# Performance work log

Hardware: AMD Instinct MI355X
Metric: run time of the kernel (lower is better)

## Reference

```python
import jax, jax.numpy as jnp
import numpy as np

NEG_SLOPE_GAT = 0.2   # GATv2 attention LeakyReLU slope (PyG default)
NEG_SLOPE_ACT = 0.01  # nn.LeakyReLU() default slope in outer module
LN_EPS = 1e-5
SOFTMAX_EPS = 1e-16   # PyG softmax denominator epsilon

B, C, N = 2, 128, 50000
H, FH = 2, 64          # heads=2, out_channels=64 -> concat dim 128
E = 800000
M = B * N


def setup_inputs() -> dict:
    key = jax.random.key(0)
    ks = jax.random.split(key, 10)
    s_in = 1.0 / np.sqrt(C)
    s_att = 1.0 / np.sqrt(FH)
    return {
        "x": jax.random.normal(ks[0], (B, C, N, 1), jnp.float32),
        "edge_index": jax.random.randint(ks[1], (2, E), 0, M, jnp.int32),
        "W_l": jax.random.normal(ks[2], (C, H * FH), jnp.float32) * s_in,
        "b_l": jnp.zeros((H * FH,), jnp.float32),
        "W_r": jax.random.normal(ks[3], (C, H * FH), jnp.float32) * s_in,
        "b_r": jnp.zeros((H * FH,), jnp.float32),
        "att": jax.random.normal(ks[4], (H, FH), jnp.float32) * s_att,
        "bias_gat": jnp.zeros((H * FH,), jnp.float32),
        "gamma": jnp.ones((H * FH,), jnp.float32),
        "beta": jnp.zeros((H * FH,), jnp.float32),
    }


def reference(x, edge_index, W_l, b_l, W_r, b_r, att, bias_gat, gamma, beta):
    Bx, Cx, Nx, _ = x.shape
    Mn = Bx * Nx
    # x.squeeze(3).permute(0,2,1).reshape(-1, C)  -> (B*N, C) node features
    xn = jnp.transpose(x[..., 0], (0, 2, 1)).reshape(Mn, Cx)
    h_l = (xn @ W_l + b_l).reshape(Mn, H, FH)   # source transform
    h_r = (xn @ W_r + b_r).reshape(Mn, H, FH)   # target transform
    src, dst = edge_index[0], edge_index[1]
    # GATv2: score = att . leaky_relu(h_l[src] + h_r[dst])
    e = jax.nn.leaky_relu(h_l[src] + h_r[dst], NEG_SLOPE_GAT)  # (E,H,FH)
    logits = jnp.einsum('ehf,hf->eh', e, att)                  # (E,H)
    # segment softmax over edges sharing a destination node
    seg_max = jax.ops.segment_max(logits, dst, num_segments=Mn)
    expl = jnp.exp(logits - seg_max[dst])
    denom = jax.ops.segment_sum(expl, dst, num_segments=Mn)
    alpha = expl / (denom[dst] + SOFTMAX_EPS)                  # (E,H)
    # weighted scatter-aggregate of source messages
    out = jax.ops.segment_sum(h_l[src] * alpha[:, :, None], dst, num_segments=Mn)
    out = out.reshape(Mn, H * FH) + bias_gat                   # concat heads + bias
    # LayerNorm(out_channels*2)
    mu = out.mean(-1, keepdims=True)
    var = out.var(-1, keepdims=True)
    out = (out - mu) * jax.lax.rsqrt(var + LN_EPS) * gamma + beta
    return jax.nn.leaky_relu(out, NEG_SLOPE_ACT)
```

## Files before the change

### kernel.cpp

```cpp
#include <hip/hip_runtime.h>
#include <hip/hip_fp16.h>
#include <cmath>

constexpr int Bc = 2;
constexpr int Cc = 128;
constexpr int Nc = 50000;
constexpr int Hh = 2;
constexpr int FHc = 64;
constexpr int HF = Hh * FHc;
constexpr int Mc = Bc * Nc;
constexpr int Ec = 800000;

constexpr int PBLK = 64;
constexpr int CHUNK = Ec / PBLK;
constexpr int KBKT = (Mc + 255) / 256;
constexpr int CAP  = 4096;
constexpr int GEMM_BLKS = (Mc + 63) / 64;

#define NSLOPE_GAT 0.2f
#define NSLOPE_ACT 0.01f
#define LN_EPS 1e-5f
#define SM_EPS 1e-16f
#define LOG2E 1.4426950408889634f


typedef __attribute__((ext_vector_type(8))) short short8;
typedef __attribute__((ext_vector_type(4))) float f32x4;
typedef _Float16 half2v __attribute__((ext_vector_type(2)));

__device__ inline unsigned short f2bf(float f) {
    union { float f; unsigned int i; } v; v.f = f;
    unsigned int r = v.i + 0x7fffu + ((v.i >> 16) & 1u);
    return (unsigned short)(r >> 16);
}

#if __has_builtin(__builtin_amdgcn_exp2f)
#define EXP2(x) __builtin_amdgcn_exp2f(x)
#else
#define EXP2(x) __expf((x) * 0.6931471805599453f)
#endif

#if __has_builtin(__builtin_amdgcn_fdot2)
#define FDOT2(a, b, c) __builtin_amdgcn_fdot2((a), (b), (c), false)
#else
__device__ inline float FDOT2(half2v a, half2v b, float c) {
    return fmaf((float)a[0], (float)b[0], fmaf((float)a[1], (float)b[1], c));
}
#endif

template <int CTRL>
__device__ inline float dpp_add_step(float x) {
    int y = __builtin_amdgcn_update_dpp(0, __builtin_bit_cast(int, x),
                                        CTRL, 0xF, 0xF, false);
    return x + __builtin_bit_cast(float, y);
}
__device__ inline float row16_sum(float x) {
    x = dpp_add_step<0x121>(x);
    x = dpp_add_step<0x122>(x);
    x = dpp_add_step<0x124>(x);
    x = dpp_add_step<0x128>(x);
    return x;
}

__global__ __launch_bounds__(256) void prep_hist(
    const float* __restrict__ Wl, const float* __restrict__ Wr,
    const float* __restrict__ att, const float* __restrict__ bias,
    const float* __restrict__ gamma, const float* __restrict__ beta,
    unsigned short* __restrict__ Wb, _Float16* __restrict__ att_h,
    float* __restrict__ bias_perm, float* __restrict__ gamma_perm,
    float* __restrict__ beta_perm,
    const int* __restrict__ ei, int* __restrict__ counts)
{
    const int tid = threadIdx.x;
    if (blockIdx.x >= 128) {
        __shared__ int hist[KBKT];
        const int p = blockIdx.x - 128;
        for (int k = tid; k < KBKT; k += 256) hist[k] = 0;
        __syncthreads();
        const int4* dsts = (const int4*)(ei + Ec + p * CHUNK);
        for (int i = tid; i < CHUNK / 4; i += 256) {
            int4 d = dsts[i];
            atomicAdd(&hist[d.x >> 8], 1);
            atomicAdd(&hist[d.y >> 8], 1);
            atomicAdd(&hist[d.z >> 8], 1);
            atomicAdd(&hist[d.w >> 8], 1);
        }
        __syncthreads();
        for (int k = tid; k < KBKT; k += 256) counts[p * KBKT + k] = hist[k];
        return;
    }
    int i = blockIdx.x * 256 + tid;
    if (blockIdx.x == 0 && tid < 128) {
        int cp = tid;
        int c = (cp & 7) * 16 + (cp >> 3);
        att_h[cp]      = (_Float16)(att[c] * LOG2E);
        bias_perm[cp]  = bias[c];
        gamma_perm[cp] = gamma[c];
        beta_perm[cp]  = beta[c];
    }
    int j = i & 7, l = (i >> 3) & 63, s = (i >> 9) & 3, nt = (i >> 11) & 7, mat = (i >> 14) & 1;
    int q = l >> 4, n15 = l & 15;
    int k = 32 * s + 8 * q + j;
    int n = 16 * nt + n15;
    const float* W = mat ? Wr : Wl;
    Wb[i] = f2bf(W[k * HF + n]);
}

__global__ __launch_bounds__(256, 3) void gemm_scatter(
    const float* __restrict__ x,
    const unsigned short* __restrict__ Wb,
    const float* __restrict__ bl, const float* __restrict__ br,
    unsigned short* __restrict__ hl, unsigned short* __restrict__ hr,
    const int* __restrict__ ei, const int* __restrict__ counts,
    unsigned int* __restrict__ pairs)
{
    __shared__ __align__(16) unsigned char smem[16384];
    const int tid = threadIdx.x;

    if (blockIdx.x < PBLK) {
        const int p = blockIdx.x;
        int* cur = (int*)smem;
        for (int k = tid; k < KBKT; k += 256) {
            int base = k * CAP;
            for (int pp = 0; pp < p; ++pp) base += counts[pp * KBKT + k];
            cur[k] = base;
        }
        __syncthreads();
        const int4* srcs = (const int4*)(ei + p * CHUNK);
        const int4* dsts = (const int4*)(ei + Ec + p * CHUNK);
        for (int i = tid; i < CHUNK / 4; i += 256) {
            int4 s = srcs[i];
            int4 d = dsts[i];
            int p0 = atomicAdd(&cur[d.x >> 8], 1);
            pairs[p0] = ((unsigned)s.x << 8) | (unsigned)(d.x & 255);
            int p1 = atomicAdd(&cur[d.y >> 8], 1);
            pairs[p1] = ((unsigned)s.y << 8) | (unsigned)(d.y & 255);
            int p2 = atomicAdd(&cur[d.z >> 8], 1);
            pairs[p2] = ((unsigned)s.z << 8) | (unsigned)(d.z & 255);
            int p3 = atomicAdd(&cur[d.w >> 8], 1);
            pairs[p3] = ((unsigned)s.w << 8) | (unsigned)(d.w & 255);
        }
        return;
    }

    unsigned char* As = smem;
    const int r0 = (blockIdx.x - PBLK) * 64;
    const int l = tid & 63, w = tid >> 6;
    const int m15 = l & 15, q = l >> 4;

    const int matw = w >> 1, ntb = 4 * (w & 1);
    const short8* __restrict__ WB = (const short8*)Wb;
    short8 bfrag[4][4];
    #pragma unroll
    for (int i = 0; i < 4; ++i)
        #pragma unroll
        for (int s = 0; s < 4; ++s)
            bfrag[i][s] = WB[(((matw * 8 + ntb + i) * 4 + s) * 64) + l];

    {
        const int lrow = tid & 63;
        const int cg   = (tid >> 6) * 4;
        const int grow = r0 + lrow;
        const unsigned int swz = (unsigned)((lrow & 7) << 4);
        const bool valid = grow < Mc;
        int b = 0, n = grow;
        if (n >= Nc) { b = 1; n -= Nc; }
        const float* xb = x + (size_t)(b * Cc) * Nc + n;
        #pragma unroll
        for (int pp = 0; pp < 8; ++pp) {
            int c = cg + 16 * pp;
            float v0 = 0.f, v1 = 0.f, v2 = 0.f, v3 = 0.f;
            if (valid) {
                const float* xp = xb + (size_t)c * Nc;
                v0 = xp[0];
                v1 = xp[Nc];
                v2 = xp[2 * (size_t)Nc];
                v3 = xp[3 * (size_t)Nc];
            }
            unsigned int d0 = (unsigned)f2bf(v0) | ((unsigned)f2bf(v1) << 16);
            unsigned int d1 = (unsigned)f2bf(v2) | ((unsigned)f2bf(v3) << 16);
            unsigned int off = (unsigned)lrow * 256 + (((unsigned)(c * 2)) ^ swz);
            *(uint2*)(As + off) = make_uint2(d0, d1);
        }
    }
    __syncthreads();

    const float* bsrc = matw ? br : bl;
    unsigned short* __restrict__ hdst = matw ? hr : hl;
    float bv[4];
    #pragma unroll
    for (int i = 0; i < 4; ++i) bv[i] = bsrc[16 * (ntb + i) + m15];

    const unsigned int rswz = (unsigned)((m15 & 7) << 4);
    #pragma unroll
    for (int mt = 0; mt < 4; ++mt) {
        short8 af[4];
        #pragma unroll
        for (int s = 0; s < 4; ++s) {
            unsigned int off = (unsigned)(16 * mt + m15) * 256 +
                               (((unsigned)(64 * s + 16 * q)) ^ rswz);
            af[s] = *(const short8*)(As + off);
        }
        f32x4 acc[4];
        #pragma unroll
        for (int i = 0; i < 4; ++i) acc[i] = (f32x4)(0.f);
        #pragma unroll
        for (int s = 0; s < 4; ++s)
            #pragma unroll
            for (int i = 0; i < 4; ++i)
                acc[i] = __builtin_amdgcn_mfma_f32_16x16x32_bf16(af[s], bfrag[i][s], acc[i], 0, 0, 0);

        #pragma unroll
        for (int reg = 0; reg < 4; ++reg) {
            int rD = r0 + 16 * mt + 4 * q + reg;
            if (rD < Mc) {
                half2v hlo = { (_Float16)(acc[0][reg] + bv[0]),
                               (_Float16)(acc[1][reg] + bv[1]) };
                half2v hhi = { (_Float16)(acc[2][reg] + bv[2]),
                               (_Float16)(acc[3][reg] + bv[3]) };
                *(uint2*)(hdst + (size_t)rD * HF + m15 * 8 + ntb) =
                    make_uint2(__builtin_bit_cast(unsigned int, hlo),
                               __builtin_bit_cast(unsigned int, hhi));
            }
        }
    }
}

__global__ __launch_bounds__(256) void bucket_csr(const unsigned int* __restrict__ pairs,
                                                  const int* __restrict__ counts,
                                                  int* __restrict__ offs,
                                                  int* __restrict__ deg,
                                                  int* __restrict__ csr_src)
{
    __shared__ int cnt[256];
    __shared__ int scn[256];
    __shared__ int cur[256];
    __shared__ int ecnt_s;
    const int b = blockIdx.x, tid = threadIdx.x;
    const int base = b * CAP;
    if (tid < 64) {
        int v = counts[tid * KBKT + b];
        #pragma unroll
        for (int o = 32; o; o >>= 1) v += __shfl_xor(v, o, 64);
        if (tid == 0) ecnt_s = v;
    }
    cnt[tid] = 0;
    __syncthreads();
    const int ecnt = ecnt_s;
    for (int i = tid; i < ecnt; i += 256)
        atomicAdd(&cnt[pairs[base + i] & 255u], 1);
    __syncthreads();
    int c = cnt[tid];
    scn[tid] = c;
    __syncthreads();
    for (int off = 1; off < 256; off <<= 1) {
        int v = (tid >= off) ? scn[tid - off] : 0;
        __syncthreads();
        scn[tid] += v;
        __syncthreads();
    }
    int excl = scn[tid] - c;
    int node = (b << 8) + tid;
    if (node < Mc) {
        offs[node] = base + excl;
        deg[node] = c;
    }
    cur[tid] = base + excl;
    __syncthreads();
    for (int i = tid; i < ecnt; i += 256) {
        unsigned pr = pairs[base + i];
        int pos = atomicAdd(&cur[pr & 255u], 1);
        csr_src[pos] = (int)(pr >> 8);
    }
}

__global__ __launch_bounds__(256) void gat_fused(
    const unsigned short* __restrict__ hl, const unsigned short* __restrict__ hr,
    const int* __restrict__ csr_src,
    const int* __restrict__ offs, const int* __restrict__ deg,
    const _Float16* __restrict__ att_h, const float* __restrict__ bias_perm,
    const float* __restrict__ gamma_perm, const float* __restrict__ beta_perm,
    float* __restrict__ out)
{
    const int wv = threadIdx.x >> 6;
    const int t  = threadIdx.x & 63;
    const int d  = blockIdx.x * 4 + wv;
    if (d >= Mc) return;
    const int off = __builtin_amdgcn_readfirstlane(offs[d]);
    const int n   = __builtin_amdgcn_readfirstlane(deg[d]);
    const int i32 = t & 31;
    const bool hiHalf = (t >= 32);
    const int g = ((i32 & 15) << 1) | (i32 >> 4);
    const unsigned int voff = 8u * (unsigned)g;

    const uint2 urr = *(const uint2*)((const char*)hr + (size_t)d * 256 + voff);
    const half2v HR01 = __builtin_bit_cast(half2v, urr.x);
    const half2v HR23 = __builtin_bit_cast(half2v, urr.y);
    const uint2 apu = *(const uint2*)((const char*)att_h + voff);
    const half2v ap01 = __builtin_bit_cast(half2v, apu.x);
    const half2v ap23 = __builtin_bit_cast(half2v, apu.y);
    const half2v slope2 = { (_Float16)NSLOPE_GAT, (_Float16)NSLOPE_GAT };

    float l = 0.f, acc0 = 0.f, acc1 = 0.f, acc2 = 0.f, acc3 = 0.f;
    const char* __restrict__ hlb = (const char*)hl;

    auto load2 = [&](int sa, int sb) -> uint2 {
        int s = hiHalf ? sb : sa;
        return *(const uint2*)(hlb + (((unsigned int)s) << 8) + voff);
    };
    auto compute = [&](uint2 u, bool tailMask) {
        half2v A01 = __builtin_bit_cast(half2v, u.x);
        half2v A23 = __builtin_bit_cast(half2v, u.y);
        half2v z01 = A01 + HR01;
        half2v z23 = A23 + HR23;
        z01 = __builtin_elementwise_max(z01, z01 * slope2);
        z23 = __builtin_elementwise_max(z23, z23 * slope2);
        float p = FDOT2(z01, ap01, FDOT2(z23, ap23, 0.f));
        p = row16_sum(p);
        float w = EXP2(p);
        if (tailMask && hiHalf) w = 0.f;
        l += w;
        acc0 = fmaf(w, (float)A01[0], acc0);
        acc1 = fmaf(w, (float)A01[1], acc1);
        acc2 = fmaf(w, (float)A23[0], acc2);
        acc3 = fmaf(w, (float)A23[1], acc3);
    };

    int i = 0;
    for (; i + 4 <= n; i += 4) {
        int s0 = csr_src[off + i];
        int s1 = csr_src[off + i + 1];
        int s2 = csr_src[off + i + 2];
        int s3 = csr_src[off + i + 3];
        uint2 u0 = load2(s0, s1);
        uint2 u1 = load2(s2, s3);
        compute(u0, false);
        compute(u1, false);
    }
    if (i + 2 <= n) {
        int s0 = csr_src[off + i];
        int s1 = csr_src[off + i + 1];
        uint2 u0 = load2(s0, s1);
        compute(u0, false);
        i += 2;
    }
    if (i < n) {
        int s0 = csr_src[off + i];
        uint2 u0 = load2(s0, s0);
        compute(u0, true);
    }

    l    += __shfl_xor(l, 32, 64);
    acc0 += __shfl_xor(acc0, 32, 64);
    acc1 += __shfl_xor(acc1, 32, 64);
    acc2 += __shfl_xor(acc2, 32, 64);
    acc3 += __shfl_xor(acc3, 32, 64);

    float inv = 1.f / (l + SM_EPS);
    const float4 bp = *(const float4*)(bias_perm + 4 * g);
    float v0 = fmaf(acc0, inv, bp.x);
    float v1 = fmaf(acc1, inv, bp.y);
    float v2 = fmaf(acc2, inv, bp.z);
    float v3 = fmaf(acc3, inv, bp.w);

    float sum = (v0 + v1) + (v2 + v3);
    #pragma unroll
    for (int o = 1; o <= 16; o <<= 1) sum += __shfl_xor(sum, o, 64);
    float mu = sum * (1.f / 128.f);
    float d0 = v0 - mu, d1 = v1 - mu, d2 = v2 - mu, d3 = v3 - mu;
    float sq = (d0 * d0 + d1 * d1) + (d2 * d2 + d3 * d3);
    #pragma unroll
    for (int o = 1; o <= 16; o <<= 1) sq += __shfl_xor(sq, o, 64);
    float rstd = rsqrtf(sq * (1.f / 128.f) + LN_EPS);

    const float4 ga = *(const float4*)(gamma_perm + 4 * g);
    const float4 be = *(const float4*)(beta_perm + 4 * g);
    float y0 = fmaf(d0 * rstd, ga.x, be.x);
    float y1 = fmaf(d1 * rstd, ga.y, be.y);
    float y2 = fmaf(d2 * rstd, ga.z, be.z);
    float y3 = fmaf(d3 * rstd, ga.w, be.w);
    y0 = fmaxf(y0, NSLOPE_ACT * y0);
    y1 = fmaxf(y1, NSLOPE_ACT * y1);
    y2 = fmaxf(y2, NSLOPE_ACT * y2);
    y3 = fmaxf(y3, NSLOPE_ACT * y3);

    if (!hiHalf) {
        const int h = g & 1, m = g >> 1;
        float* op = out + (size_t)d * HF + 64 * h + m;
        op[0]  = y0;
        op[16] = y1;
        op[32] = y2;
        op[48] = y3;
    }
}

extern "C" void kernel_launch(void* const* d_in, const int* in_sizes, int n_in,
                              void* d_out, int out_size, void* d_ws, size_t ws_size,
                              hipStream_t stream) {
    const float* x     = (const float*)d_in[0];
    const int*   ei    = (const int*)d_in[1];
    const float* Wl    = (const float*)d_in[2];
    const float* bl    = (const float*)d_in[3];
    const float* Wr    = (const float*)d_in[4];
    const float* br    = (const float*)d_in[5];
    const float* att   = (const float*)d_in[6];
    const float* bias  = (const float*)d_in[7];
    const float* gamma = (const float*)d_in[8];
    const float* beta  = (const float*)d_in[9];
    float* out = (float*)d_out;

    char* ws = (char*)d_ws;
    unsigned short* hl = (unsigned short*)ws; ws += (size_t)Mc * HF * 2;
    unsigned short* hr = (unsigned short*)ws; ws += (size_t)Mc * HF * 2;
    unsigned short* Wb = (unsigned short*)ws; ws += 32768 * 2;
    _Float16* att_h   = (_Float16*)ws; ws += 512;
    float* bias_perm  = (float*)ws; ws += 128 * sizeof(float);
    float* gamma_perm = (float*)ws; ws += 128 * sizeof(float);
    float* beta_perm  = (float*)ws; ws += 128 * sizeof(float);
    int* deg = (int*)ws;        ws += (size_t)Mc * sizeof(int);
    int* offs = (int*)ws;       ws += (size_t)Mc * sizeof(int);
    int* counts = (int*)ws;     ws += (size_t)PBLK * KBKT * sizeof(int);
    unsigned int* pairs = (unsigned int*)ws; ws += (size_t)KBKT * CAP * 4;
    int* csr_src = (int*)ws;    ws += (size_t)KBKT * CAP * 4;

    prep_hist<<<128 + PBLK, 256, 0, stream>>>(Wl, Wr, att, bias, gamma, beta,
                                              Wb, att_h, bias_perm, gamma_perm,
                                              beta_perm, ei, counts);
    gemm_scatter<<<PBLK + GEMM_BLKS, 256, 0, stream>>>(x, Wb, bl, br, hl, hr,
                                                       ei, counts, pairs);
    bucket_csr<<<KBKT, 256, 0, stream>>>(pairs, counts, offs, deg, csr_src);
    gat_fused<<<(Mc + 3) / 4, 256, 0, stream>>>(hl, hr, csr_src, offs, deg,
                                                att_h, bias_perm, gamma_perm,
                                                beta_perm, out);
}
```

Baseline: 214.1 us.

## Fuse bucket CSR build into GAT aggregation via LDS and split GEMM per matrix

The bucket-sort kernel and the per-node GAT aggregation kernel become one 1024-thread-per-bucket kernel. It builds the per-bucket CSR source list in shared memory and then processes the bucket's 256 destination nodes, 16 per wave. This removes one launch and the global round-trip of csr_src, offs and deg. Separately, the GEMM grid is doubled so each block computes only one of the two projection matrices, with fewer accumulator registers, and the occupancy hint rises to 4. The trade-off is that only 391 large blocks handle the aggregation, which may reduce parallelism and leave load imbalance across buckets, and the x tile is loaded twice.

```diff
diff --git a/kernel.cpp b/kernel.cpp
--- a/kernel.cpp
+++ b/kernel.cpp
@@ -106,7 +106,7 @@
     Wb[i] = f2bf(W[k * HF + n]);
 }
 
-__global__ __launch_bounds__(256, 3) void gemm_scatter(
+__global__ __launch_bounds__(256, 4) void gemm_scatter(
     const float* __restrict__ x,
     const unsigned short* __restrict__ Wb,
     const float* __restrict__ bl, const float* __restrict__ br,
@@ -144,15 +144,17 @@
     }
 
     unsigned char* As = smem;
-    const int r0 = (blockIdx.x - PBLK) * 64;
+    const int gb = blockIdx.x - PBLK;
+    const int matw = gb & 1;
+    const int r0 = (gb >> 1) * 64;
     const int l = tid & 63, w = tid >> 6;
     const int m15 = l & 15, q = l >> 4;
 
-    const int matw = w >> 1, ntb = 4 * (w & 1);
+    const int ntb = 2 * w;
     const short8* __restrict__ WB = (const short8*)Wb;
-    short8 bfrag[4][4];
+    short8 bfrag[2][4];
     #pragma unroll
-    for (int i = 0; i < 4; ++i)
+    for (int i = 0; i < 2; ++i)
         #pragma unroll
         for (int s = 0; s < 4; ++s)
             bfrag[i][s] = WB[(((matw * 8 + ntb + i) * 4 + s) * 64) + l];
@@ -187,9 +189,9 @@
 
     const float* bsrc = matw ? br : bl;
     unsigned short* __restrict__ hdst = matw ? hr : hl;
-    float bv[4];
-    #pragma unroll
-    for (int i = 0; i < 4; ++i) bv[i] = bsrc[16 * (ntb + i) + m15];
+    float bv[2];
+    bv[0] = bsrc[16 * ntb + m15];
+    bv[1] = bsrc[16 * (ntb + 1) + m15];
 
     const unsigned int rswz = (unsigned)((m15 & 7) << 4);
     #pragma unroll
@@ -201,196 +203,189 @@
                                (((unsigned)(64 * s + 16 * q)) ^ rswz);
             af[s] = *(const short8*)(As + off);
         }
-        f32x4 acc[4];
-        #pragma unroll
-        for (int i = 0; i < 4; ++i) acc[i] = (f32x4)(0.f);
-        #pragma unroll
-        for (int s = 0; s < 4; ++s)
-            #pragma unroll
-            for (int i = 0; i < 4; ++i)
-                acc[i] = __builtin_amdgcn_mfma_f32_16x16x32_bf16(af[s], bfrag[i][s], acc[i], 0, 0, 0);
+        f32x4 acc[2];
+        acc[0] = (f32x4)(0.f);
+        acc[1] = (f32x4)(0.f);
+        #pragma unroll
+        for (int s = 0; s < 4; ++s) {
+            acc[0] = __builtin_amdgcn_mfma_f32_16x16x32_bf16(af[s], bfrag[0][s], acc[0], 0, 0, 0);
+            acc[1] = __builtin_amdgcn_mfma_f32_16x16x32_bf16(af[s], bfrag[1][s], acc[1], 0, 0, 0);
+        }
 
         #pragma unroll
         for (int reg = 0; reg < 4; ++reg) {
             int rD = r0 + 16 * mt + 4 * q + reg;
             if (rD < Mc) {
-                half2v hlo = { (_Float16)(acc[0][reg] + bv[0]),
-                               (_Float16)(acc[1][reg] + bv[1]) };
-                half2v hhi = { (_Float16)(acc[2][reg] + bv[2]),
-                               (_Float16)(acc[3][reg] + bv[3]) };
-                *(uint2*)(hdst + (size_t)rD * HF + m15 * 8 + ntb) =
-                    make_uint2(__builtin_bit_cast(unsigned int, hlo),
-                               __builtin_bit_cast(unsigned int, hhi));
+                half2v hv = { (_Float16)(acc[0][reg] + bv[0]),
+                              (_Float16)(acc[1][reg] + bv[1]) };
+                *(unsigned int*)(hdst + (size_t)rD * HF + m15 * 8 + ntb) =
+                    __builtin_bit_cast(unsigned int, hv);
             }
         }
     }
 }
 
-__global__ __launch_bounds__(256) void bucket_csr(const unsigned int* __restrict__ pairs,
-                                                  const int* __restrict__ counts,
-                                                  int* __restrict__ offs,
-                                                  int* __restrict__ deg,
-                                                  int* __restrict__ csr_src)
+__global__ __launch_bounds__(1024) void gat_bucket(
+    const unsigned short* __restrict__ hl, const unsigned short* __restrict__ hr,
+    const unsigned int* __restrict__ pairs, const int* __restrict__ counts,
+    const _Float16* __restrict__ att_h, const float* __restrict__ bias_perm,
+    const float* __restrict__ gamma_perm, const float* __restrict__ beta_perm,
+    float* __restrict__ out)
 {
     __shared__ int cnt[256];
     __shared__ int scn[256];
     __shared__ int cur[256];
+    __shared__ int elds[CAP];
     __shared__ int ecnt_s;
     const int b = blockIdx.x, tid = threadIdx.x;
     const int base = b * CAP;
+
     if (tid < 64) {
         int v = counts[tid * KBKT + b];
         #pragma unroll
         for (int o = 32; o; o >>= 1) v += __shfl_xor(v, o, 64);
         if (tid == 0) ecnt_s = v;
     }
-    cnt[tid] = 0;
+    if (tid < 256) cnt[tid] = 0;
     __syncthreads();
     const int ecnt = ecnt_s;
-    for (int i = tid; i < ecnt; i += 256)
+    for (int i = tid; i < ecnt; i += 1024)
         atomicAdd(&cnt[pairs[base + i] & 255u], 1);
     __syncthreads();
-    int c = cnt[tid];
-    scn[tid] = c;
+    int c = 0;
+    if (tid < 256) { c = cnt[tid]; scn[tid] = c; }
     __syncthreads();
     for (int off = 1; off < 256; off <<= 1) {
-        int v = (tid >= off) ? scn[tid - off] : 0;
+        int v = 0;
+        if (tid < 256 && tid >= off) v = scn[tid - off];
         __syncthreads();
-        scn[tid] += v;
+        if (tid < 256) scn[tid] += v;
         __syncthreads();
     }
-    int excl = scn[tid] - c;
-    int node = (b << 8) + tid;
-    if (node < Mc) {
-        offs[node] = base + excl;
-        deg[node] = c;
-    }
-    cur[tid] = base + excl;
-    __syncthreads();
-    for (int i = tid; i < ecnt; i += 256) {
+    if (tid < 256) cur[tid] = scn[tid] - c;
+    __syncthreads();
+    for (int i = tid; i < ecnt; i += 1024) {
         unsigned pr = pairs[base + i];
         int pos = atomicAdd(&cur[pr & 255u], 1);
-        csr_src[pos] = (int)(pr >> 8);
-    }
-}
-
-__global__ __launch_bounds__(256) void gat_fused(
-    const unsigned short* __restrict__ hl, const unsigned short* __restrict__ hr,
-    const int* __restrict__ csr_src,
-    const int* __restrict__ offs, const int* __restrict__ deg,
-    const _Float16* __restrict__ att_h, const float* __restrict__ bias_perm,
-    const float* __restrict__ gamma_perm, const float* __restrict__ beta_perm,
-    float* __restrict__ out)
-{
-    const int wv = threadIdx.x >> 6;
-    const int t  = threadIdx.x & 63;
-    const int d  = blockIdx.x * 4 + wv;
-    if (d >= Mc) return;
-    const int off = __builtin_amdgcn_readfirstlane(offs[d]);
-    const int n   = __builtin_amdgcn_readfirstlane(deg[d]);
+        elds[pos] = (int)(pr >> 8);
+    }
+    __syncthreads();
+
+    const int wv = tid >> 6;
+    const int t  = tid & 63;
     const int i32 = t & 31;
     const bool hiHalf = (t >= 32);
     const int g = ((i32 & 15) << 1) | (i32 >> 4);
     const unsigned int voff = 8u * (unsigned)g;
 
-    const uint2 urr = *(const uint2*)((const char*)hr + (size_t)d * 256 + voff);
-    const half2v HR01 = __builtin_bit_cast(half2v, urr.x);
-    const half2v HR23 = __builtin_bit_cast(half2v, urr.y);
     const uint2 apu = *(const uint2*)((const char*)att_h + voff);
     const half2v ap01 = __builtin_bit_cast(half2v, apu.x);
     const half2v ap23 = __builtin_bit_cast(half2v, apu.y);
     const half2v slope2 = { (_Float16)NSLOPE_GAT, (_Float16)NSLOPE_GAT };
-
-    float l = 0.f, acc0 = 0.f, acc1 = 0.f, acc2 = 0.f, acc3 = 0.f;
-    const char* __restrict__ hlb = (const char*)hl;
-
-    auto load2 = [&](int sa, int sb) -> uint2 {
-        int s = hiHalf ? sb : sa;
-        return *(const uint2*)(hlb + (((unsigned int)s) << 8) + voff);
-    };
-    auto compute = [&](uint2 u, bool tailMask) {
-        half2v A01 = __builtin_bit_cast(half2v, u.x);
-        half2v A23 = __builtin_bit_cast(half2v, u.y);
-        half2v z01 = A01 + HR01;
-        half2v z23 = A23 + HR23;
-        z01 = __builtin_elementwise_max(z01, z01 * slope2);
-        z23 = __builtin_elementwise_max(z23, z23 * slope2);
-        float p = FDOT2(z01, ap01, FDOT2(z23, ap23, 0.f));
-        p = row16_sum(p);
-        float w = EXP2(p);
-        if (tailMask && hiHalf) w = 0.f;
-        l += w;
-        acc0 = fmaf(w, (float)A01[0], acc0);
-        acc1 = fmaf(w, (float)A01[1], acc1);
-        acc2 = fmaf(w, (float)A23[0], acc2);
-        acc3 = fmaf(w, (float)A23[1], acc3);
-    };
-
-    int i = 0;
-    for (; i + 4 <= n; i += 4) {
-        int s0 = csr_src[off + i];
-        int s1 = csr_src[off + i + 1];
-        int s2 = csr_src[off + i + 2];
-        int s3 = csr_src[off + i + 3];
-        uint2 u0 = load2(s0, s1);
-        uint2 u1 = load2(s2, s3);
-        compute(u0, false);
-        compute(u1, false);
-    }
-    if (i + 2 <= n) {
-        int s0 = csr_src[off + i];
-        int s1 = csr_src[off + i + 1];
-        uint2 u0 = load2(s0, s1);
-        compute(u0, false);
-        i += 2;
-    }
-    if (i < n) {
-        int s0 = csr_src[off + i];
-        uint2 u0 = load2(s0, s0);
-        compute(u0, true);
-    }
-
-    l    += __shfl_xor(l, 32, 64);
-    acc0 += __shfl_xor(acc0, 32, 64);
-    acc1 += __shfl_xor(acc1, 32, 64);
-    acc2 += __shfl_xor(acc2, 32, 64);
-    acc3 += __shfl_xor(acc3, 32, 64);
-
-    float inv = 1.f / (l + SM_EPS);
     const float4 bp = *(const float4*)(bias_perm + 4 * g);
-    float v0 = fmaf(acc0, inv, bp.x);
-    float v1 = fmaf(acc1, inv, bp.y);
-    float v2 = fmaf(acc2, inv, bp.z);
-    float v3 = fmaf(acc3, inv, bp.w);
-
-    float sum = (v0 + v1) + (v2 + v3);
-    #pragma unroll
-    for (int o = 1; o <= 16; o <<= 1) sum += __shfl_xor(sum, o, 64);
-    float mu = sum * (1.f / 128.f);
-    float d0 = v0 - mu, d1 = v1 - mu, d2 = v2 - mu, d3 = v3 - mu;
-    float sq = (d0 * d0 + d1 * d1) + (d2 * d2 + d3 * d3);
-    #pragma unroll
-    for (int o = 1; o <= 16; o <<= 1) sq += __shfl_xor(sq, o, 64);
-    float rstd = rsqrtf(sq * (1.f / 128.f) + LN_EPS);
-
     const float4 ga = *(const float4*)(gamma_perm + 4 * g);
     const float4 be = *(const float4*)(beta_perm + 4 * g);
-    float y0 = fmaf(d0 * rstd, ga.x, be.x);
-    float y1 = fmaf(d1 * rstd, ga.y, be.y);
-    float y2 = fmaf(d2 * rstd, ga.z, be.z);
-    float y3 = fmaf(d3 * rstd, ga.w, be.w);
-    y0 = fmaxf(y0, NSLOPE_ACT * y0);
-    y1 = fmaxf(y1, NSLOPE_ACT * y1);
-    y2 = fmaxf(y2, NSLOPE_ACT * y2);
-    y3 = fmaxf(y3, NSLOPE_ACT * y3);
-
-    if (!hiHalf) {
-        const int h = g & 1, m = g >> 1;
-        float* op = out + (size_t)d * HF + 64 * h + m;
-        op[0]  = y0;
-        op[16] = y1;
-        op[32] = y2;
-        op[48] = y3;
+    const char* __restrict__ hlb = (const char*)hl;
+
+    for (int j = 0; j < 16; ++j) {
+        const int ln = wv * 16 + j;
+        const int d = (b << 8) + ln;
+        if (d >= Mc) break;
+
+        const int n    = __builtin_amdgcn_readfirstlane(cnt[ln]);
+        const int offl = __builtin_amdgcn_readfirstlane(scn[ln]) - n;
+
+        const uint2 urr = *(const uint2*)((const char*)hr + (size_t)d * 256 + voff);
+        const half2v HR01 = __builtin_bit_cast(half2v, urr.x);
+        const half2v HR23 = __builtin_bit_cast(half2v, urr.y);
+
+        float l = 0.f, acc0 = 0.f, acc1 = 0.f, acc2 = 0.f, acc3 = 0.f;
+
+        auto load2 = [&](int sa, int sb) -> uint2 {
+            int s = hiHalf ? sb : sa;
+            return *(const uint2*)(hlb + (((unsigned int)s) << 8) + voff);
+        };
+        auto compute = [&](uint2 u, bool tailMask) {
+            half2v A01 = __builtin_bit_cast(half2v, u.x);
+            half2v A23 = __builtin_bit_cast(half2v, u.y);
+            half2v z01 = A01 + HR01;
+            half2v z23 = A23 + HR23;
+            z01 = __builtin_elementwise_max(z01, z01 * slope2);
+            z23 = __builtin_elementwise_max(z23, z23 * slope2);
+            float p = FDOT2(z01, ap01, FDOT2(z23, ap23, 0.f));
+            p = row16_sum(p);
+            float w = EXP2(p);
+            if (tailMask && hiHalf) w = 0.f;
+            l += w;
+            acc0 = fmaf(w, (float)A01[0], acc0);
+            acc1 = fmaf(w, (float)A01[1], acc1);
+            acc2 = fmaf(w, (float)A23[0], acc2);
+            acc3 = fmaf(w, (float)A23[1], acc3);
+        };
+
+        int i = 0;
+        for (; i + 4 <= n; i += 4) {
+            int s0 = elds[offl + i];
+            int s1 = elds[offl + i + 1];
+            int s2 = elds[offl + i + 2];
+            int s3 = elds[offl + i + 3];
+            uint2 u0 = load2(s0, s1);
+            uint2 u1 = load2(s2, s3);
+            compute(u0, false);
+            compute(u1, false);
+        }
+        if (i + 2 <= n) {
+            int s0 = elds[offl + i];
+            int s1 = elds[offl + i + 1];
+            uint2 u0 = load2(s0, s1);
+            compute(u0, false);
+            i += 2;
+        }
+        if (i < n) {
+            int s0 = elds[offl + i];
+            uint2 u0 = load2(s0, s0);
+            compute(u0, true);
+        }
+
+        l    += __shfl_xor(l, 32, 64);
+        acc0 += __shfl_xor(acc0, 32, 64);
+        acc1 += __shfl_xor(acc1, 32, 64);
+        acc2 += __shfl_xor(acc2, 32, 64);
+        acc3 += __shfl_xor(acc3, 32, 64);
+
+        float inv = 1.f / (l + SM_EPS);
+        float v0 = fmaf(acc0, inv, bp.x);
+        float v1 = fmaf(acc1, inv, bp.y);
+        float v2 = fmaf(acc2, inv, bp.z);
+        float v3 = fmaf(acc3, inv, bp.w);
+
+        float sum = (v0 + v1) + (v2 + v3);
+        #pragma unroll
+        for (int o = 1; o <= 16; o <<= 1) sum += __shfl_xor(sum, o, 64);
+        float mu = sum * (1.f / 128.f);
+        float d0 = v0 - mu, d1 = v1 - mu, d2 = v2 - mu, d3 = v3 - mu;
+        float sq = (d0 * d0 + d1 * d1) + (d2 * d2 + d3 * d3);
+        #pragma unroll
+        for (int o = 1; o <= 16; o <<= 1) sq += __shfl_xor(sq, o, 64);
+        float rstd = rsqrtf(sq * (1.f / 128.f) + LN_EPS);
+
+        float y0 = fmaf(d0 * rstd, ga.x, be.x);
+        float y1 = fmaf(d1 * rstd, ga.y, be.y);
+        float y2 = fmaf(d2 * rstd, ga.z, be.z);
+        float y3 = fmaf(d3 * rstd, ga.w, be.w);
+        y0 = fmaxf(y0, NSLOPE_ACT * y0);
+        y1 = fmaxf(y1, NSLOPE_ACT * y1);
+        y2 = fmaxf(y2, NSLOPE_ACT * y2);
+        y3 = fmaxf(y3, NSLOPE_ACT * y3);
+
+        if (!hiHalf) {
+            const int h = g & 1, m = g >> 1;
+            float* op = out + (size_t)d * HF + 64 * h + m;
+            op[0]  = y0;
+            op[16] = y1;
+            op[32] = y2;
+            op[48] = y3;
+        }
     }
 }
 
@@ -417,19 +412,14 @@
     float* bias_perm  = (float*)ws; ws += 128 * sizeof(float);
     float* gamma_perm = (float*)ws; ws += 128 * sizeof(float);
     float* beta_perm  = (float*)ws; ws += 128 * sizeof(float);
-    int* deg = (int*)ws;        ws += (size_t)Mc * sizeof(int);
-    int* offs = (int*)ws;       ws += (size_t)Mc * sizeof(int);
     int* counts = (int*)ws;     ws += (size_t)PBLK * KBKT * sizeof(int);
     unsigned int* pairs = (unsigned int*)ws; ws += (size_t)KBKT * CAP * 4;
-    int* csr_src = (int*)ws;    ws += (size_t)KBKT * CAP * 4;
 
     prep_hist<<<128 + PBLK, 256, 0, stream>>>(Wl, Wr, att, bias, gamma, beta,
                                               Wb, att_h, bias_perm, gamma_perm,
                                               beta_perm, ei, counts);
-    gemm_scatter<<<PBLK + GEMM_BLKS, 256, 0, stream>>>(x, Wb, bl, br, hl, hr,
-                                                       ei, counts, pairs);
-    bucket_csr<<<KBKT, 256, 0, stream>>>(pairs, counts, offs, deg, csr_src);
-    gat_fused<<<(Mc + 3) / 4, 256, 0, stream>>>(hl, hr, csr_src, offs, deg,
-                                                att_h, bias_perm, gamma_perm,
-                                                beta_perm, out);
-}
+    gemm_scatter<<<PBLK + 2 * GEMM_BLKS, 256, 0, stream>>>(x, Wb, bl, br, hl, hr,
+                                                           ei, counts, pairs);
+    gat_bucket<<<KBKT, 1024, 0, stream>>>(hl, hr, pairs, counts, att_h,
+                                          bias_perm, gamma_perm, beta_perm, out);
+}
```

Result: slower. 224.9 us (+5.1%).

## Process four edges per wave with 16 lanes each using 16-byte gathers

Applied to the files above, without the earlier changes.

Reorganizes the fused GAT aggregation so each wavefront handles four edges per iteration, with 16 lanes per edge loading 16 bytes each, instead of two edges with 32 lanes loading 8 bytes. A single predicated loop replaces the unrolled main and tail paths, and partial sums are merged across the four edge rows with shuffles. This is meant to cut loop iterations and the number of memory instructions per gathered row, and to spread the final stores across all lanes. In exchange each lane holds twice as many accumulators, and the layout assumes the permuted hr/att/bias layout matches the new lane mapping.

```diff
diff --git a/kernel.cpp b/kernel.cpp
--- a/kernel.cpp
+++ b/kernel.cpp
@@ -288,110 +288,118 @@
     if (d >= Mc) return;
     const int off = __builtin_amdgcn_readfirstlane(offs[d]);
     const int n   = __builtin_amdgcn_readfirstlane(deg[d]);
-    const int i32 = t & 31;
-    const bool hiHalf = (t >= 32);
-    const int g = ((i32 & 15) << 1) | (i32 >> 4);
-    const unsigned int voff = 8u * (unsigned)g;
-
-    const uint2 urr = *(const uint2*)((const char*)hr + (size_t)d * 256 + voff);
+    const int erow = t >> 4;
+    const int i16  = t & 15;
+    const unsigned int voff = 16u * (unsigned)i16;
+
+    const uint4 urr = *(const uint4*)((const char*)hr + (size_t)d * 256 + voff);
     const half2v HR01 = __builtin_bit_cast(half2v, urr.x);
     const half2v HR23 = __builtin_bit_cast(half2v, urr.y);
-    const uint2 apu = *(const uint2*)((const char*)att_h + voff);
+    const half2v HR45 = __builtin_bit_cast(half2v, urr.z);
+    const half2v HR67 = __builtin_bit_cast(half2v, urr.w);
+    const uint4 apu = *(const uint4*)((const char*)att_h + voff);
     const half2v ap01 = __builtin_bit_cast(half2v, apu.x);
     const half2v ap23 = __builtin_bit_cast(half2v, apu.y);
+    const half2v ap45 = __builtin_bit_cast(half2v, apu.z);
+    const half2v ap67 = __builtin_bit_cast(half2v, apu.w);
     const half2v slope2 = { (_Float16)NSLOPE_GAT, (_Float16)NSLOPE_GAT };
 
-    float l = 0.f, acc0 = 0.f, acc1 = 0.f, acc2 = 0.f, acc3 = 0.f;
+    float l0 = 0.f, l1 = 0.f;
+    float acc0 = 0.f, acc1 = 0.f, acc2 = 0.f, acc3 = 0.f;
+    float acc4 = 0.f, acc5 = 0.f, acc6 = 0.f, acc7 = 0.f;
     const char* __restrict__ hlb = (const char*)hl;
 
-    auto load2 = [&](int sa, int sb) -> uint2 {
-        int s = hiHalf ? sb : sa;
-        return *(const uint2*)(hlb + (((unsigned int)s) << 8) + voff);
-    };
-    auto compute = [&](uint2 u, bool tailMask) {
+    for (int i = 0; i < n; i += 4) {
+        const int idx = i + erow;
+        const bool valid = idx < n;
+        const int s = csr_src[off + (valid ? idx : n - 1)];
+        const uint4 u = *(const uint4*)(hlb + (((unsigned int)s) << 8) + voff);
         half2v A01 = __builtin_bit_cast(half2v, u.x);
         half2v A23 = __builtin_bit_cast(half2v, u.y);
+        half2v A45 = __builtin_bit_cast(half2v, u.z);
+        half2v A67 = __builtin_bit_cast(half2v, u.w);
         half2v z01 = A01 + HR01;
         half2v z23 = A23 + HR23;
+        half2v z45 = A45 + HR45;
+        half2v z67 = A67 + HR67;
         z01 = __builtin_elementwise_max(z01, z01 * slope2);
         z23 = __builtin_elementwise_max(z23, z23 * slope2);
-        float p = FDOT2(z01, ap01, FDOT2(z23, ap23, 0.f));
-        p = row16_sum(p);
-        float w = EXP2(p);
-        if (tailMask && hiHalf) w = 0.f;
-        l += w;
-        acc0 = fmaf(w, (float)A01[0], acc0);
-        acc1 = fmaf(w, (float)A01[1], acc1);
-        acc2 = fmaf(w, (float)A23[0], acc2);
-        acc3 = fmaf(w, (float)A23[1], acc3);
-    };
-
-    int i = 0;
-    for (; i + 4 <= n; i += 4) {
-        int s0 = csr_src[off + i];
-        int s1 = csr_src[off + i + 1];
-        int s2 = csr_src[off + i + 2];
-        int s3 = csr_src[off + i + 3];
-        uint2 u0 = load2(s0, s1);
-        uint2 u1 = load2(s2, s3);
-        compute(u0, false);
-        compute(u1, false);
-    }
-    if (i + 2 <= n) {
-        int s0 = csr_src[off + i];
-        int s1 = csr_src[off + i + 1];
-        uint2 u0 = load2(s0, s1);
-        compute(u0, false);
-        i += 2;
-    }
-    if (i < n) {
-        int s0 = csr_src[off + i];
-        uint2 u0 = load2(s0, s0);
-        compute(u0, true);
-    }
-
-    l    += __shfl_xor(l, 32, 64);
-    acc0 += __shfl_xor(acc0, 32, 64);
-    acc1 += __shfl_xor(acc1, 32, 64);
-    acc2 += __shfl_xor(acc2, 32, 64);
-    acc3 += __shfl_xor(acc3, 32, 64);
-
-    float inv = 1.f / (l + SM_EPS);
-    const float4 bp = *(const float4*)(bias_perm + 4 * g);
-    float v0 = fmaf(acc0, inv, bp.x);
-    float v1 = fmaf(acc1, inv, bp.y);
-    float v2 = fmaf(acc2, inv, bp.z);
-    float v3 = fmaf(acc3, inv, bp.w);
-
-    float sum = (v0 + v1) + (v2 + v3);
-    #pragma unroll
-    for (int o = 1; o <= 16; o <<= 1) sum += __shfl_xor(sum, o, 64);
+        z45 = __builtin_elementwise_max(z45, z45 * slope2);
+        z67 = __builtin_elementwise_max(z67, z67 * slope2);
+        float p0 = FDOT2(z01, ap01, FDOT2(z23, ap23, 0.f));
+        float p1 = FDOT2(z45, ap45, FDOT2(z67, ap67, 0.f));
+        p0 = row16_sum(p0);
+        p1 = row16_sum(p1);
+        float w0 = EXP2(p0);
+        float w1 = EXP2(p1);
+        if (!valid) { w0 = 0.f; w1 = 0.f; }
+        l0 += w0;
+        l1 += w1;
+        acc0 = fmaf(w0, (float)A01[0], acc0);
+        acc1 = fmaf(w0, (float)A01[1], acc1);
+        acc2 = fmaf(w0, (float)A23[0], acc2);
+        acc3 = fmaf(w0, (float)A23[1], acc3);
+        acc4 = fmaf(w1, (float)A45[0], acc4);
+        acc5 = fmaf(w1, (float)A45[1], acc5);
+        acc6 = fmaf(w1, (float)A67[0], acc6);
+        acc7 = fmaf(w1, (float)A67[1], acc7);
+    }
+
+#define MRG(v) { v += __shfl_xor(v, 16, 64); v += __shfl_xor(v, 32, 64); }
+    MRG(l0) MRG(l1)
+    MRG(acc0) MRG(acc1) MRG(acc2) MRG(acc3)
+    MRG(acc4) MRG(acc5) MRG(acc6) MRG(acc7)
+#undef MRG
+
+    const float inv0 = 1.f / (l0 + SM_EPS);
+    const float inv1 = 1.f / (l1 + SM_EPS);
+    const float4 bpA = *(const float4*)(bias_perm + 8 * i16);
+    const float4 bpB = *(const float4*)(bias_perm + 8 * i16 + 4);
+    float v0 = fmaf(acc0, inv0, bpA.x);
+    float v1 = fmaf(acc1, inv0, bpA.y);
+    float v2 = fmaf(acc2, inv0, bpA.z);
+    float v3 = fmaf(acc3, inv0, bpA.w);
+    float v4 = fmaf(acc4, inv1, bpB.x);
+    float v5 = fmaf(acc5, inv1, bpB.y);
+    float v6 = fmaf(acc6, inv1, bpB.z);
+    float v7 = fmaf(acc7, inv1, bpB.w);
+
+    float sum = ((v0 + v1) + (v2 + v3)) + ((v4 + v5) + (v6 + v7));
+    sum = row16_sum(sum);
     float mu = sum * (1.f / 128.f);
     float d0 = v0 - mu, d1 = v1 - mu, d2 = v2 - mu, d3 = v3 - mu;
-    float sq = (d0 * d0 + d1 * d1) + (d2 * d2 + d3 * d3);
-    #pragma unroll
-    for (int o = 1; o <= 16; o <<= 1) sq += __shfl_xor(sq, o, 64);
+    float d4 = v4 - mu, d5 = v5 - mu, d6 = v6 - mu, d7 = v7 - mu;
+    float sq = ((d0 * d0 + d1 * d1) + (d2 * d2 + d3 * d3)) +
+               ((d4 * d4 + d5 * d5) + (d6 * d6 + d7 * d7));
+    sq = row16_sum(sq);
     float rstd = rsqrtf(sq * (1.f / 128.f) + LN_EPS);
 
-    const float4 ga = *(const float4*)(gamma_perm + 4 * g);
-    const float4 be = *(const float4*)(beta_perm + 4 * g);
-    float y0 = fmaf(d0 * rstd, ga.x, be.x);
-    float y1 = fmaf(d1 * rstd, ga.y, be.y);
-    float y2 = fmaf(d2 * rstd, ga.z, be.z);
-    float y3 = fmaf(d3 * rstd, ga.w, be.w);
+    const float4 gaA = *(const float4*)(gamma_perm + 8 * i16);
+    const float4 gaB = *(const float4*)(gamma_perm + 8 * i16 + 4);
+    const float4 beA = *(const float4*)(beta_perm + 8 * i16);
+    const float4 beB = *(const float4*)(beta_perm + 8 * i16 + 4);
+    float y0 = fmaf(d0 * rstd, gaA.x, beA.x);
+    float y1 = fmaf(d1 * rstd, gaA.y, beA.y);
+    float y2 = fmaf(d2 * rstd, gaA.z, beA.z);
+    float y3 = fmaf(d3 * rstd, gaA.w, beA.w);
+    float y4 = fmaf(d4 * rstd, gaB.x, beB.x);
+    float y5 = fmaf(d5 * rstd, gaB.y, beB.y);
+    float y6 = fmaf(d6 * rstd, gaB.z, beB.z);
+    float y7 = fmaf(d7 * rstd, gaB.w, beB.w);
     y0 = fmaxf(y0, NSLOPE_ACT * y0);
     y1 = fmaxf(y1, NSLOPE_ACT * y1);
     y2 = fmaxf(y2, NSLOPE_ACT * y2);
     y3 = fmaxf(y3, NSLOPE_ACT * y3);
-
-    if (!hiHalf) {
-        const int h = g & 1, m = g >> 1;
-        float* op = out + (size_t)d * HF + 64 * h + m;
-        op[0]  = y0;
-        op[16] = y1;
-        op[32] = y2;
-        op[48] = y3;
-    }
+    y4 = fmaxf(y4, NSLOPE_ACT * y4);
+    y5 = fmaxf(y5, NSLOPE_ACT * y5);
+    y6 = fmaxf(y6, NSLOPE_ACT * y6);
+    y7 = fmaxf(y7, NSLOPE_ACT * y7);
+
+    float ya = (erow == 0) ? y0 : (erow == 1) ? y2 : (erow == 2) ? y4 : y6;
+    float yb = (erow == 0) ? y1 : (erow == 1) ? y3 : (erow == 2) ? y5 : y7;
+    float* op = out + (size_t)d * HF + i16;
+    op[16 * (2 * erow)]     = ya;
+    op[16 * (2 * erow + 1)] = yb;
 }
 
 extern "C" void kernel_launch(void* const* d_in, const int* in_sizes, int n_in,
```

Measured after the change: 221.9 us. 3.6% more time.
